# Performance work log

Measured on AMD Instinct MI355X. Metric: run time of the kernel, lower is better.

Reference implementation:

```python
import jax, jax.numpy as jnp
import numpy as np

NUM_WORDS = 35000
EMBED_DIM = 100
MAX_LEN = 80
BATCH = 2048
UNITS = 512


def setup_inputs() -> dict:
    key = jax.random.key(0)
    ks = jax.random.split(key, 7)
    inputs = jax.random.randint(ks[0], (BATCH, MAX_LEN), 0, NUM_WORDS)
    emb_table = jax.random.normal(ks[1], (NUM_WORDS, EMBED_DIM), jnp.float32) * 0.05
    W_xh = jax.random.normal(ks[2], (EMBED_DIM, UNITS), jnp.float32) * (1.0 / np.sqrt(EMBED_DIM))
    W_hh = jax.random.normal(ks[3], (UNITS, UNITS), jnp.float32) * (1.0 / np.sqrt(UNITS))
    b_h = jnp.zeros((UNITS,), jnp.float32)
    W_out = jax.random.normal(ks[4], (UNITS, 1), jnp.float32) * (1.0 / np.sqrt(UNITS))
    b_out = jnp.zeros((1,), jnp.float32)
    return {"inputs": inputs, "emb_table": emb_table, "W_xh": W_xh,
            "W_hh": W_hh, "b_h": b_h, "W_out": W_out, "b_out": b_out}


def reference(inputs, emb_table, W_xh, W_hh, b_h, W_out, b_out):
    # Embedding lookup: [B, T, D]
    x = emb_table[inputs]
    # Precompute input projection for all timesteps (batched GEMM): [B, T, U]
    xw = jnp.einsum('btd,du->btu', x, W_xh) + b_h
    h0 = jnp.zeros((inputs.shape[0], W_hh.shape[0]), x.dtype)

    def step(h, xt):
        # SimpleRNNCell (inference, dropout off): h' = tanh(x@W_xh + b + h@W_hh)
        h_new = jnp.tanh(xt + h @ W_hh)
        return h_new, None

    # scan over time axis; carry only the [B, U] hidden state
    h_last, _ = jax.lax.scan(step, h0, jnp.swapaxes(xw, 0, 1))
    logits = h_last @ W_out + b_out  # [B, 1]
    return jax.nn.sigmoid(logits)
```

## Files before the change

kernel.cpp:

```cpp
#include <hip/hip_runtime.h>
#include <hip/hip_bf16.h>


#define T_LEN   80
#define EMB_D   100
#define UNITS   512
#define ROWS    16
#define NBLK    128
#define NTHR    512
#define NT      4
#define KSH     16
#define KSX     4
#define RKS     6

typedef __bf16 bf16x8 __attribute__((ext_vector_type(8)));
typedef float  f32x4  __attribute__((ext_vector_type(4)));

__device__ __forceinline__ float fast_tanh(float x) {
    float e = __builtin_amdgcn_exp2f(x * 2.8853900817779268f);
    return 1.0f - 2.0f * __builtin_amdgcn_rcpf(1.0f + e);
}

__global__ void prep_kernel(const float* __restrict__ Whh,
                            const float* __restrict__ Wxh,
                            __bf16* __restrict__ Wt, __bf16* __restrict__ Xt) {
    __shared__ float tile[32][33];
    const int tx = threadIdx.x & 31, ty = threadIdx.x >> 5;
    const int b = blockIdx.x;
    if (b < 256) {
        const int k0 = (b & 15) * 32, n0 = (b >> 4) * 32;
        #pragma unroll
        for (int i = 0; i < 4; ++i)
            tile[ty + 8 * i][tx] = Whh[(k0 + ty + 8 * i) * UNITS + n0 + tx];
        __syncthreads();
        #pragma unroll
        for (int i = 0; i < 4; ++i) {
            const int n = ty + 8 * i;
            Wt[(n0 + n) * UNITS + k0 + tx] = (__bf16)tile[tx][n];
        }
    } else {
        const int bb = b - 256;
        const int k0 = (bb & 3) * 32, n0 = (bb >> 2) * 32;
        #pragma unroll
        for (int i = 0; i < 4; ++i) {
            const int k = k0 + ty + 8 * i;
            tile[ty + 8 * i][tx] = (k < EMB_D) ? Wxh[k * UNITS + n0 + tx] : 0.0f;
        }
        __syncthreads();
        #pragma unroll
        for (int i = 0; i < 4; ++i) {
            const int n = ty + 8 * i;
            Xt[(n0 + n) * 128 + k0 + tx] = (__bf16)tile[tx][n];
        }
    }
}

__global__ __launch_bounds__(NTHR, 1)
void rnn_kernel(const int*   __restrict__ inputs,
                const float* __restrict__ emb,
                const float* __restrict__ bh,
                const float* __restrict__ Wout,
                const float* __restrict__ bout,
                const __bf16* __restrict__ Wt,
                const __bf16* __restrict__ Xt,
                float*       __restrict__ out)
{
    __shared__ alignas(16) __bf16 hbuf[2][16 * UNITS];
    __shared__ alignas(16) __bf16 xbuf[2][16 * 128];

    const int tid  = threadIdx.x;
    const int wave = tid >> 6;
    const int lane = tid & 63;
    const int q    = lane >> 4;
    const int ln   = lane & 15;
    const int e7   = ln & 7;
    const int qa   = q ^ (e7 & 3);
    const int kx   = e7 >> 2;
    const int q8   = q << 3;
    const int r0   = blockIdx.x * ROWS;

    int coff[NT], cxff[NT];
    float bhv[NT];
    #pragma unroll
    for (int nt = 0; nt < NT; ++nt) {
        const int c = (wave << 6) + (nt << 4) + ln;
        coff[nt] = c * UNITS;
        cxff[nt] = c * 128;
        bhv[nt]  = bh[c];
    }

    bf16x8 whh[RKS][NT];
    bf16x8 wxh[KSX][NT];
    #pragma unroll
    for (int nt = 0; nt < NT; ++nt) {
        #pragma unroll
        for (int ks = 0; ks < RKS; ++ks)
            whh[ks][nt] = *(const bf16x8*)(Wt + coff[nt] + (ks << 5) + q8);
        #pragma unroll
        for (int ks = 0; ks < KSX; ++ks)
            wxh[ks][nt] = *(const bf16x8*)(Xt + cxff[nt] + (ks << 5) + q8);
    }

    {
        int4 z; z.x = z.y = z.z = z.w = 0;
        int4* hp = (int4*)&hbuf[0][0];
        #pragma unroll
        for (int i = 0; i < 4; ++i) hp[tid + i * NTHR] = z;
        int4* xp = (int4*)&xbuf[0][0];
        xp[tid] = z;
    }
    __syncthreads();

    auto stage = [&](int t, __bf16* xb) {
        #pragma unroll
        for (int rr = 0; rr < 2; ++rr) {
            const int r = wave + (rr << 3);
            const int idxv = inputs[(r0 + r) * T_LEN + t];
            const float* er = emb + (size_t)idxv * EMB_D;
            const int k0 = lane;
            xb[(r << 7) + ((((k0 >> 3) ^ (r & 7)) << 3) | (k0 & 7))] = (__bf16)er[k0];
            const int k1 = lane + 64;
            if (k1 < EMB_D)
                xb[(r << 7) + ((((k1 >> 3) ^ (r & 7)) << 3) | (k1 & 7))] = (__bf16)er[k1];
        }
    };

    auto step = [&](const __bf16* hb_r, const __bf16* xb_r, __bf16* hb_w) {
        bf16x8 sB[2][NT];
        #pragma unroll
        for (int nt = 0; nt < NT; ++nt)
            sB[0][nt] = *(const bf16x8*)(Wt + coff[nt] + (RKS << 5) + q8);
        #pragma unroll
        for (int nt = 0; nt < NT; ++nt)
            sB[1][nt] = *(const bf16x8*)(Wt + coff[nt] + ((RKS + 1) << 5) + q8);

        f32x4 acc[NT];
        #pragma unroll
        for (int nt = 0; nt < NT; ++nt) {
            f32x4 a = {bhv[nt], bhv[nt], bhv[nt], bhv[nt]};
            acc[nt] = a;
        }

        const int xbase = (ln << 7) + (qa << 3);
        #pragma unroll
        for (int ks = 0; ks < KSX; ++ks) {
            bf16x8 a = *(const bf16x8*)&xb_r[xbase + ((ks ^ kx) << 5)];
            #pragma unroll
            for (int nt = 0; nt < NT; ++nt)
                acc[nt] = __builtin_amdgcn_mfma_f32_16x16x32_bf16(a, wxh[ks][nt], acc[nt], 0, 0, 0);
        }
        const int hbase = (ln << 9) + (qa << 3);
        #pragma unroll
        for (int ks = 0; ks < RKS; ++ks) {
            bf16x8 a = *(const bf16x8*)&hb_r[hbase + ((ks ^ kx) << 5)];
            #pragma unroll
            for (int nt = 0; nt < NT; ++nt)
                acc[nt] = __builtin_amdgcn_mfma_f32_16x16x32_bf16(a, whh[ks][nt], acc[nt], 0, 0, 0);
        }
        #pragma unroll
        for (int ks = RKS; ks < KSH; ++ks) {
            const int s = (ks - RKS) & 1;
            bf16x8 a = *(const bf16x8*)&hb_r[hbase + ((ks ^ kx) << 5)];
            #pragma unroll
            for (int nt = 0; nt < NT; ++nt)
                acc[nt] = __builtin_amdgcn_mfma_f32_16x16x32_bf16(a, sB[s][nt], acc[nt], 0, 0, 0);
            if (ks + 2 < KSH) {
                #pragma unroll
                for (int nt = 0; nt < NT; ++nt)
                    sB[s][nt] = *(const bf16x8*)(Wt + coff[nt] + ((ks + 2) << 5) + q8);
            }
        }
        #pragma unroll
        for (int nt = 0; nt < NT; ++nt) {
            const int cc = (wave << 3) + (nt << 1) + (ln >> 3);
            #pragma unroll
            for (int i = 0; i < 4; ++i) {
                const int row = (q << 2) + i;
                hb_w[(row << 9) + (((cc ^ (row & 7)) << 3) | (ln & 7))] =
                    (__bf16)fast_tanh(acc[nt][i]);
            }
        }
    };

    stage(0, xbuf[0]);
    __syncthreads();

    #pragma unroll 1
    for (int t = 0; t < T_LEN; t += 2) {
        stage(t + 1, xbuf[1]);
        step(hbuf[0], xbuf[0], hbuf[1]);
        __syncthreads();
        if (t + 2 < T_LEN) stage(t + 2, xbuf[0]);
        step(hbuf[1], xbuf[1], hbuf[0]);
        __syncthreads();
    }

    #pragma unroll
    for (int rr = 0; rr < 2; ++rr) {
        const int m = wave + (rr << 3);
        const bf16x8 hv = *(const bf16x8*)&hbuf[0][(m << 9) + ((lane ^ wave) << 3)];
        float s = 0.0f;
        #pragma unroll
        for (int j = 0; j < 8; ++j)
            s += (float)hv[j] * Wout[(lane << 3) + j];
        #pragma unroll
        for (int off = 32; off > 0; off >>= 1)
            s += __shfl_down(s, off, 64);
        if (lane == 0) {
            const float logit = s + bout[0];
            out[r0 + m] = __builtin_amdgcn_rcpf(
                1.0f + __builtin_amdgcn_exp2f(-logit * 1.4426950408889634f));
        }
    }
}

extern "C" void kernel_launch(void* const* d_in, const int* in_sizes, int n_in,
                              void* d_out, int out_size, void* d_ws, size_t ws_size,
                              hipStream_t stream) {
    __bf16* Wt = (__bf16*)d_ws;
    __bf16* Xt = Wt + UNITS * UNITS;
    prep_kernel<<<dim3(320), dim3(256), 0, stream>>>(
        (const float*)d_in[3],
        (const float*)d_in[2],
        Wt, Xt);
    rnn_kernel<<<dim3(NBLK), dim3(NTHR), 0, stream>>>(
        (const int*)d_in[0],
        (const float*)d_in[1],
        (const float*)d_in[4],
        (const float*)d_in[5],
        (const float*)d_in[6],
        Wt, Xt,
        (float*)d_out);
}
```

Measured before the change: 1.106 ms.

## Stream all weights from fragment-ordered global layout with 4-deep rolling prefetch

The prep kernel now writes W_hh and W_xh in MFMA fragment order, so each wave's per-k-slice B operands sit contiguously and lanes load coalesced 16-byte chunks. The RNN kernel no longer keeps 10 k-slices of weights resident in registers. Every timestep it streams all 20 k-slices (x part plus h part) through a 4-stage rolling register buffer, prefetching slice kk+4 while slice kk's MFMAs run. This frees registers, since launch_bounds no longer forces one block per SM. The cost is more L2 weight traffic per step, and the wrap-around prefetch for the next step is issued before the barrier.

```diff
diff --git a/kernel.cpp b/kernel.cpp
--- a/kernel.cpp
+++ b/kernel.cpp
@@ -11,7 +11,7 @@
 #define NT      4
 #define KSH     16
 #define KSX     4
-#define RKS     6
+#define KTOT    (KSH + KSX)
 
 typedef __bf16 bf16x8 __attribute__((ext_vector_type(8)));
 typedef float  f32x4  __attribute__((ext_vector_type(4)));
@@ -23,46 +23,36 @@
 
 __global__ void prep_kernel(const float* __restrict__ Whh,
                             const float* __restrict__ Wxh,
-                            __bf16* __restrict__ Wt, __bf16* __restrict__ Xt) {
-    __shared__ float tile[32][33];
-    const int tx = threadIdx.x & 31, ty = threadIdx.x >> 5;
-    const int b = blockIdx.x;
-    if (b < 256) {
-        const int k0 = (b & 15) * 32, n0 = (b >> 4) * 32;
-        #pragma unroll
-        for (int i = 0; i < 4; ++i)
-            tile[ty + 8 * i][tx] = Whh[(k0 + ty + 8 * i) * UNITS + n0 + tx];
-        __syncthreads();
-        #pragma unroll
-        for (int i = 0; i < 4; ++i) {
-            const int n = ty + 8 * i;
-            Wt[(n0 + n) * UNITS + k0 + tx] = (__bf16)tile[tx][n];
-        }
+                            __bf16* __restrict__ FW, __bf16* __restrict__ FX) {
+    const int f = blockIdx.x * 256 + threadIdx.x;
+    if (f < 32768) {
+        const int lane = f & 63, nt = (f >> 6) & 3, ks = (f >> 8) & 15, w = f >> 12;
+        const int c  = (w << 6) + (nt << 4) + (lane & 15);
+        const int kb = (ks << 5) + ((lane >> 4) << 3);
+        __bf16* d = FW + (size_t)f * 8;
+        #pragma unroll
+        for (int j = 0; j < 8; ++j)
+            d[j] = (__bf16)Whh[(kb + j) * UNITS + c];
     } else {
-        const int bb = b - 256;
-        const int k0 = (bb & 3) * 32, n0 = (bb >> 2) * 32;
-        #pragma unroll
-        for (int i = 0; i < 4; ++i) {
-            const int k = k0 + ty + 8 * i;
-            tile[ty + 8 * i][tx] = (k < EMB_D) ? Wxh[k * UNITS + n0 + tx] : 0.0f;
-        }
-        __syncthreads();
-        #pragma unroll
-        for (int i = 0; i < 4; ++i) {
-            const int n = ty + 8 * i;
-            Xt[(n0 + n) * 128 + k0 + tx] = (__bf16)tile[tx][n];
-        }
-    }
-}
-
-__global__ __launch_bounds__(NTHR, 1)
+        const int f2 = f - 32768;
+        const int lane = f2 & 63, nt = (f2 >> 6) & 3, ks = (f2 >> 8) & 3, w = f2 >> 10;
+        const int c  = (w << 6) + (nt << 4) + (lane & 15);
+        const int kb = (ks << 5) + ((lane >> 4) << 3);
+        __bf16* d = FX + (size_t)f2 * 8;
+        #pragma unroll
+        for (int j = 0; j < 8; ++j)
+            d[j] = (kb + j < EMB_D) ? (__bf16)Wxh[(kb + j) * UNITS + c] : (__bf16)0.0f;
+    }
+}
+
+__global__ __launch_bounds__(NTHR)
 void rnn_kernel(const int*   __restrict__ inputs,
                 const float* __restrict__ emb,
                 const float* __restrict__ bh,
                 const float* __restrict__ Wout,
                 const float* __restrict__ bout,
-                const __bf16* __restrict__ Wt,
-                const __bf16* __restrict__ Xt,
+                const __bf16* __restrict__ FW,
+                const __bf16* __restrict__ FX,
                 float*       __restrict__ out)
 {
     __shared__ alignas(16) __bf16 hbuf[2][16 * UNITS];
@@ -76,30 +66,29 @@
     const int e7   = ln & 7;
     const int qa   = q ^ (e7 & 3);
     const int kx   = e7 >> 2;
-    const int q8   = q << 3;
     const int r0   = blockIdx.x * ROWS;
 
-    int coff[NT], cxff[NT];
     float bhv[NT];
     #pragma unroll
-    for (int nt = 0; nt < NT; ++nt) {
-        const int c = (wave << 6) + (nt << 4) + ln;
-        coff[nt] = c * UNITS;
-        cxff[nt] = c * 128;
-        bhv[nt]  = bh[c];
-    }
-
-    bf16x8 whh[RKS][NT];
-    bf16x8 wxh[KSX][NT];
-    #pragma unroll
-    for (int nt = 0; nt < NT; ++nt) {
-        #pragma unroll
-        for (int ks = 0; ks < RKS; ++ks)
-            whh[ks][nt] = *(const bf16x8*)(Wt + coff[nt] + (ks << 5) + q8);
-        #pragma unroll
-        for (int ks = 0; ks < KSX; ++ks)
-            wxh[ks][nt] = *(const bf16x8*)(Xt + cxff[nt] + (ks << 5) + q8);
-    }
+    for (int nt = 0; nt < NT; ++nt)
+        bhv[nt] = bh[(wave << 6) + (nt << 4) + ln];
+
+    bf16x8 sB[4][NT];
+
+    auto pf = [&](int kk, bf16x8* dst) {
+        if (kk < KSX) {
+            const __bf16* p = FX + ((wave << 13) + (kk << 11) + (lane << 3));
+            #pragma unroll
+            for (int nt = 0; nt < NT; ++nt)
+                dst[nt] = *(const bf16x8*)(p + (nt << 9));
+        } else {
+            const int ks = kk - KSX;
+            const __bf16* p = FW + ((wave << 15) + (ks << 11) + (lane << 3));
+            #pragma unroll
+            for (int nt = 0; nt < NT; ++nt)
+                dst[nt] = *(const bf16x8*)(p + (nt << 9));
+        }
+    };
 
     {
         int4 z; z.x = z.y = z.z = z.w = 0;
@@ -126,14 +115,6 @@
     };
 
     auto step = [&](const __bf16* hb_r, const __bf16* xb_r, __bf16* hb_w) {
-        bf16x8 sB[2][NT];
-        #pragma unroll
-        for (int nt = 0; nt < NT; ++nt)
-            sB[0][nt] = *(const bf16x8*)(Wt + coff[nt] + (RKS << 5) + q8);
-        #pragma unroll
-        for (int nt = 0; nt < NT; ++nt)
-            sB[1][nt] = *(const bf16x8*)(Wt + coff[nt] + ((RKS + 1) << 5) + q8);
-
         f32x4 acc[NT];
         #pragma unroll
         for (int nt = 0; nt < NT; ++nt) {
@@ -142,34 +123,22 @@
         }
 
         const int xbase = (ln << 7) + (qa << 3);
-        #pragma unroll
-        for (int ks = 0; ks < KSX; ++ks) {
-            bf16x8 a = *(const bf16x8*)&xb_r[xbase + ((ks ^ kx) << 5)];
-            #pragma unroll
-            for (int nt = 0; nt < NT; ++nt)
-                acc[nt] = __builtin_amdgcn_mfma_f32_16x16x32_bf16(a, wxh[ks][nt], acc[nt], 0, 0, 0);
-        }
         const int hbase = (ln << 9) + (qa << 3);
-        #pragma unroll
-        for (int ks = 0; ks < RKS; ++ks) {
-            bf16x8 a = *(const bf16x8*)&hb_r[hbase + ((ks ^ kx) << 5)];
-            #pragma unroll
-            for (int nt = 0; nt < NT; ++nt)
-                acc[nt] = __builtin_amdgcn_mfma_f32_16x16x32_bf16(a, whh[ks][nt], acc[nt], 0, 0, 0);
-        }
-        #pragma unroll
-        for (int ks = RKS; ks < KSH; ++ks) {
-            const int s = (ks - RKS) & 1;
-            bf16x8 a = *(const bf16x8*)&hb_r[hbase + ((ks ^ kx) << 5)];
+
+        #pragma unroll
+        for (int kk = 0; kk < KTOT; ++kk) {
+            bf16x8 a;
+            if (kk < KSX)
+                a = *(const bf16x8*)&xb_r[xbase + ((kk ^ kx) << 5)];
+            else
+                a = *(const bf16x8*)&hb_r[hbase + (((kk - KSX) ^ kx) << 5)];
+            const int s = kk & 3;
             #pragma unroll
             for (int nt = 0; nt < NT; ++nt)
                 acc[nt] = __builtin_amdgcn_mfma_f32_16x16x32_bf16(a, sB[s][nt], acc[nt], 0, 0, 0);
-            if (ks + 2 < KSH) {
-                #pragma unroll
-                for (int nt = 0; nt < NT; ++nt)
-                    sB[s][nt] = *(const bf16x8*)(Wt + coff[nt] + ((ks + 2) << 5) + q8);
-            }
-        }
+            pf((kk + 4) % KTOT, sB[s]);
+        }
+
         #pragma unroll
         for (int nt = 0; nt < NT; ++nt) {
             const int cc = (wave << 3) + (nt << 1) + (ln >> 3);
@@ -181,6 +150,8 @@
             }
         }
     };
+
+    pf(0, sB[0]); pf(1, sB[1]); pf(2, sB[2]); pf(3, sB[3]);
 
     stage(0, xbuf[0]);
     __syncthreads();
@@ -217,18 +188,18 @@
 extern "C" void kernel_launch(void* const* d_in, const int* in_sizes, int n_in,
                               void* d_out, int out_size, void* d_ws, size_t ws_size,
                               hipStream_t stream) {
-    __bf16* Wt = (__bf16*)d_ws;
-    __bf16* Xt = Wt + UNITS * UNITS;
-    prep_kernel<<<dim3(320), dim3(256), 0, stream>>>(
+    __bf16* FW = (__bf16*)d_ws;
+    __bf16* FX = FW + UNITS * UNITS;
+    prep_kernel<<<dim3(160), dim3(256), 0, stream>>>(
         (const float*)d_in[3],
         (const float*)d_in[2],
-        Wt, Xt);
+        FW, FX);
     rnn_kernel<<<dim3(NBLK), dim3(NTHR), 0, stream>>>(
         (const int*)d_in[0],
         (const float*)d_in[1],
         (const float*)d_in[4],
         (const float*)d_in[5],
         (const float*)d_in[6],
-        Wt, Xt,
+        FW, FX,
         (float*)d_out);
 }
```

After: 1.429 ms. 1.29x slower.
